# Kernel tuning notes

Hardware: AMD Instinct MI355X
Metric: run time of the kernel (lower is better)

## Reference

```python
import jax, jax.numpy as jnp
import numpy as np

EPS = 1e-5

def conv1x1(x, W, b):
    # x: [B,Cin,H,W], W: [Cout,Cin], b: [Cout] -> [B,Cout,H,W]
    return jnp.einsum('oc,bchw->bohw', W, x) + b[None, :, None, None]

def setup_inputs() -> dict:
    key = jax.random.key(0)
    ks = jax.random.split(key, 12)
    C, Ci = 256, 128
    B, Hh, Wh, Hl, Wl = 8, 32, 32, 64, 64
    sc = 1.0 / np.sqrt(C)
    sci = 1.0 / np.sqrt(Ci)
    return {
        'x_high': jax.random.normal(ks[0], (B, C, Hh, Wh), jnp.float32),
        'x_low':  jax.random.normal(ks[1], (B, C, Hl, Wl), jnp.float32),
        'Wg': jax.random.normal(ks[2], (Ci, C), jnp.float32) * sc,
        'bg': jax.random.normal(ks[3], (Ci,), jnp.float32) * 0.01,
        'Wt': jax.random.normal(ks[4], (Ci, C), jnp.float32) * sc,
        'bt': jax.random.normal(ks[5], (Ci,), jnp.float32) * 0.01,
        'Wp': jax.random.normal(ks[6], (Ci, C), jnp.float32) * sc,
        'bp': jax.random.normal(ks[7], (Ci,), jnp.float32) * 0.01,
        'Wz': jax.random.normal(ks[8], (C, Ci), jnp.float32) * sci,
        'bz': jax.random.normal(ks[9], (C,), jnp.float32) * 0.01,
        'gamma': jnp.ones((C,), jnp.float32),
        'beta': jnp.zeros((C,), jnp.float32),
    }

def reference(x_high, x_low, Wg, bg, Wt, bt, Wp, bp, Wz, bz, gamma, beta):
    B, C, Hl, Wl = x_low.shape
    Ci = Wg.shape[0]
    Nh = x_high.shape[2] * x_high.shape[3]
    Nl = Hl * Wl
    # 1x1 conv projections (pure channel GEMMs)
    g_x = conv1x1(x_high, Wg, bg).reshape(B, Ci, Nh).transpose(0, 2, 1)    # [B,Nh,Ci]
    theta_x = conv1x1(x_low, Wt, bt).reshape(B, Ci, Nl).transpose(0, 2, 1) # [B,Nl,Ci]
    phi_x = conv1x1(x_high, Wp, bp).reshape(B, Ci, Nh)                     # [B,Ci,Nh]
    # unnormalized attention (no softmax), scaled by number of key positions
    f = jnp.matmul(theta_x, phi_x)            # [B,Nl,Nh]
    y = jnp.matmul(f / Nh, g_x)               # [B,Nl,Ci]
    y = y.transpose(0, 2, 1).reshape(B, Ci, Hl, Wl)
    # W_z: 1x1 conv then GroupNorm(num_groups=1) -> layernorm over (C,H,W) per sample
    z = conv1x1(y, Wz, bz)                    # [B,C,Hl,Wl]
    mu = jnp.mean(z, axis=(1, 2, 3), keepdims=True)
    var = jnp.var(z, axis=(1, 2, 3), keepdims=True)
    z = (z - mu) * jax.lax.rsqrt(var + EPS)
    z = z * gamma[None, :, None, None] + beta[None, :, None, None]
    return z
```

## Files before the change

### kernel.cpp

```cpp
#include <hip/hip_runtime.h>
#include <hip/hip_bf16.h>

typedef __attribute__((ext_vector_type(8))) short bf16x8;
typedef __attribute__((ext_vector_type(4))) float f32x4;
typedef __attribute__((ext_vector_type(4))) unsigned short us4;
typedef __attribute__((ext_vector_type(8))) unsigned short us8;

#define MFMA(a, b, c) __builtin_amdgcn_mfma_f32_16x16x32_bf16(a, b, c, 0, 0, 0)

__device__ inline unsigned short f2bf(float f) {
  unsigned u = __builtin_bit_cast(unsigned, f);
  u += 0x7FFF + ((u >> 16) & 1);
  return (unsigned short)(u >> 16);
}
__device__ inline float bf2f(unsigned short s) {
  unsigned u = ((unsigned)s) << 16;
  return __builtin_bit_cast(float, u);
}
__device__ inline void gll16(const unsigned short* gsrc, unsigned short* ldst) {
  __builtin_amdgcn_global_load_lds(
      (const __attribute__((address_space(1))) unsigned int*)gsrc,
      (__attribute__((address_space(3))) unsigned int*)ldst, 16, 0, 0);
}

__global__ __launch_bounds__(256) void trans_cn(
    const float* __restrict__ src, unsigned short* __restrict__ dst, int N) {
  __shared__ float Ts[64][65];
  const int b = blockIdx.x, c0 = blockIdx.y * 64, n0 = blockIdx.z * 64;
  const int t = threadIdx.x;
  #pragma unroll
  for (int j = 0; j < 4; ++j) {
    int slot = t + j * 256;
    int c = slot >> 4, q = slot & 15;
    float4 v = *(const float4*)&src[((size_t)(b * 256 + c0 + c)) * N + n0 + q * 4];
    Ts[c][q * 4 + 0] = v.x; Ts[c][q * 4 + 1] = v.y;
    Ts[c][q * 4 + 2] = v.z; Ts[c][q * 4 + 3] = v.w;
  }
  __syncthreads();
  #pragma unroll
  for (int rr = 0; rr < 2; ++rr) {
    int n = rr * 32 + (t >> 3), gq = t & 7;
    us8 u;
    #pragma unroll
    for (int k = 0; k < 8; ++k) u[k] = f2bf(Ts[gq * 8 + k][n]);
    *(us8*)&dst[((size_t)(b * N + n0 + n)) * 256 + c0 + gq * 8] = u;
  }
}

__global__ __launch_bounds__(256) void cvt_w2(
    const float* __restrict__ A, const float* __restrict__ B,
    unsigned short* __restrict__ Ab, unsigned short* __restrict__ Bb) {
  int i = blockIdx.x * 256 + threadIdx.x;
  float4 a = *(const float4*)&A[i * 4];
  float4 b = *(const float4*)&B[i * 4];
  us4 ua, ub;
  ua[0] = f2bf(a.x); ua[1] = f2bf(a.y); ua[2] = f2bf(a.z); ua[3] = f2bf(a.w);
  ub[0] = f2bf(b.x); ub[1] = f2bf(b.y); ub[2] = f2bf(b.z); ub[3] = f2bf(b.w);
  *(us4*)&Ab[i * 4] = ua;
  *(us4*)&Bb[i * 4] = ub;
}

__global__ __launch_bounds__(256) void proj_mfma(
    const unsigned short* __restrict__ xhT,
    const unsigned short* __restrict__ Wpb, const float* __restrict__ bp,
    const unsigned short* __restrict__ Wgb, const float* __restrict__ bg,
    unsigned short* __restrict__ phi,
    unsigned short* __restrict__ gg) {
  __shared__ unsigned short Bs[64 * 256];
  __shared__ unsigned short As[2][128 * 64];
  const int b = blockIdx.x, n0 = blockIdx.y * 64;
  const int t = threadIdx.x, lane = t & 63;
  const int wid = t >> 6, wr = wid >> 1, wc = wid & 1;
  #pragma unroll
  for (int j = 0; j < 8; ++j) {
    int slot = t + j * 256;
    int r = slot >> 5, gq = slot & 31;
    gll16(xhT + ((size_t)(b * 1024 + n0 + r)) * 256 + (gq ^ (r & 7)) * 8,
          Bs + slot * 8);
  }
  f32x4 accP[4][2] = {};
  f32x4 accG[4][2] = {};
  for (int kt = 0; kt < 4; ++kt) {
    #pragma unroll
    for (int p = 0; p < 2; ++p) {
      const unsigned short* W = p ? Wgb : Wpb;
      #pragma unroll
      for (int j = 0; j < 4; ++j) {
        int slot = t + j * 256;
        int r = slot >> 3, gq = slot & 7;
        gll16(W + (size_t)r * 256 + kt * 64 + (gq ^ (r & 7)) * 8,
              As[p] + slot * 8);
      }
    }
    __syncthreads();
    #pragma unroll
    for (int ks = 0; ks < 2; ++ks) {
      bf16x8 bfr[2];
      #pragma unroll
      for (int fm = 0; fm < 2; ++fm) {
        int r = wc * 32 + fm * 16 + (lane & 15);
        int gc = kt * 8 + ks * 4 + (lane >> 4);
        bfr[fm] = *(const bf16x8*)&Bs[r * 256 + (gc ^ (r & 7)) * 8];
      }
      #pragma unroll
      for (int fo = 0; fo < 4; ++fo) {
        int r = wr * 64 + fo * 16 + (lane & 15);
        int ga = ks * 4 + (lane >> 4);
        bf16x8 ap = *(const bf16x8*)&As[0][r * 64 + (ga ^ (r & 7)) * 8];
        bf16x8 ag = *(const bf16x8*)&As[1][r * 64 + (ga ^ (r & 7)) * 8];
        accP[fo][0] = MFMA(ap, bfr[0], accP[fo][0]);
        accP[fo][1] = MFMA(ap, bfr[1], accP[fo][1]);
        accG[fo][0] = MFMA(ag, bfr[0], accG[fo][0]);
        accG[fo][1] = MFMA(ag, bfr[1], accG[fo][1]);
      }
    }
    __syncthreads();
  }
  #pragma unroll
  for (int fo = 0; fo < 4; ++fo) {
    #pragma unroll
    for (int q = 0; q < 4; ++q) {
      int i = wr * 64 + fo * 16 + (lane >> 4) * 4 + q;
      float vp = bp[i], vg = bg[i];
      #pragma unroll
      for (int fm = 0; fm < 2; ++fm) {
        int n = n0 + wc * 32 + fm * 16 + (lane & 15);
        size_t off = ((size_t)(b * 128 + i)) * 1024 + n;
        phi[off] = f2bf(accP[fo][fm][q] + vp);
        gg[off]  = f2bf(accG[fo][fm][q] + vg);
      }
    }
  }
}

__global__ __launch_bounds__(256) void mpart_mfma(
    const unsigned short* __restrict__ phi, const unsigned short* __restrict__ gg,
    float* __restrict__ Mpart) {
  __shared__ unsigned short ps[128 * 128];
  __shared__ unsigned short gs[128 * 128];
  const int b = blockIdx.x, kc = blockIdx.y;
  const int t = threadIdx.x, lane = t & 63;
  const int wid = t >> 6, wr = wid >> 1, wc = wid & 1;
  #pragma unroll
  for (int j = 0; j < 8; ++j) {
    int slot = t + j * 256;
    int r = slot >> 4, gq = slot & 15;
    size_t src = ((size_t)(b * 128 + r)) * 1024 + kc * 128 + (gq ^ (r & 7)) * 8;
    gll16(phi + src, ps + slot * 8);
    gll16(gg + src, gs + slot * 8);
  }
  __syncthreads();
  f32x4 acc[4][4] = {};
  #pragma unroll
  for (int ks = 0; ks < 4; ++ks) {
    bf16x8 av[4], bv[4];
    #pragma unroll
    for (int f = 0; f < 4; ++f) {
      int ra = wr * 64 + f * 16 + (lane & 15);
      int rb = wc * 64 + f * 16 + (lane & 15);
      int gc = ks * 4 + (lane >> 4);
      av[f] = *(const bf16x8*)&ps[ra * 128 + (gc ^ (ra & 7)) * 8];
      bv[f] = *(const bf16x8*)&gs[rb * 128 + (gc ^ (rb & 7)) * 8];
    }
    #pragma unroll
    for (int i = 0; i < 4; ++i)
      #pragma unroll
      for (int j2 = 0; j2 < 4; ++j2)
        acc[i][j2] = MFMA(av[i], bv[j2], acc[i][j2]);
  }
  float* mp = Mpart + ((size_t)(b * 8 + kc)) * 128 * 128;
  #pragma unroll
  for (int i = 0; i < 4; ++i)
    #pragma unroll
    for (int q = 0; q < 4; ++q) {
      int ii = wr * 64 + i * 16 + (lane >> 4) * 4 + q;
      #pragma unroll
      for (int j2 = 0; j2 < 4; ++j2) {
        int jj = wc * 64 + j2 * 16 + (lane & 15);
        mp[ii * 128 + jj] = acc[i][j2][q];
      }
    }
}

__global__ __launch_bounds__(256) void mreduce(
    const float* __restrict__ Mpart, float* __restrict__ M) {
  int i4 = blockIdx.x * 256 + threadIdx.x;
  int b = i4 >> 12, r4 = i4 & 4095;
  const float4* p = (const float4*)Mpart + (size_t)b * 8 * 4096 + r4;
  float4 s = {0.f, 0.f, 0.f, 0.f};
  #pragma unroll
  for (int kc = 0; kc < 8; ++kc) {
    float4 v = p[(size_t)kc * 4096];
    s.x += v.x; s.y += v.y; s.z += v.z; s.w += v.w;
  }
  const float sc = 1.0f / 1024.0f;
  s.x *= sc; s.y *= sc; s.z *= sc; s.w *= sc;
  ((float4*)M)[i4] = s;
}

__global__ __launch_bounds__(256) void mk_K(
    const float* __restrict__ M, const float* __restrict__ Wz,
    float* __restrict__ K) {
  const int b = blockIdx.x, o0 = blockIdx.y * 32;
  const int t = threadIdx.x;
  const int i = t & 127, og = (t >> 7) * 16;
  float acc[16] = {};
  const float* mrow = M + ((size_t)(b * 128 + i)) * 128;
  for (int j = 0; j < 128; j += 4) {
    float4 m4 = *(const float4*)&mrow[j];
    #pragma unroll
    for (int o = 0; o < 16; ++o) {
      float4 w4 = *(const float4*)&Wz[(o0 + og + o) * 128 + j];
      acc[o] += m4.x * w4.x + m4.y * w4.y + m4.z * w4.z + m4.w * w4.w;
    }
  }
  #pragma unroll
  for (int o = 0; o < 16; ++o)
    K[((size_t)(b * 256 + o0 + og + o)) * 128 + i] = acc[o];
}

__global__ __launch_bounds__(256) void mk_W2(
    const float* __restrict__ K, const float* __restrict__ Wt,
    const float* __restrict__ bt, const float* __restrict__ bz,
    unsigned short* __restrict__ W2b, float* __restrict__ b2) {
  __shared__ float Ks[32 * 128];
  const int b = blockIdx.x, o0 = blockIdx.y * 32;
  const int t = threadIdx.x;
  #pragma unroll
  for (int k = 0; k < 4; ++k) {
    int f = t + k * 256;
    int o = f >> 5, q = (f & 31) << 2;
    *(float4*)&Ks[o * 128 + q] = *(const float4*)&K[((size_t)(b * 256 + o0 + o)) * 128 + q];
  }
  __syncthreads();
  const int c = t;
  float acc[32] = {};
  for (int i = 0; i < 128; i += 4) {
    float w0 = Wt[(i + 0) * 256 + c];
    float w1 = Wt[(i + 1) * 256 + c];
    float w2 = Wt[(i + 2) * 256 + c];
    float w3 = Wt[(i + 3) * 256 + c];
    #pragma unroll
    for (int o = 0; o < 32; ++o) {
      float4 k4 = *(const float4*)&Ks[o * 128 + i];
      acc[o] += k4.x * w0 + k4.y * w1 + k4.z * w2 + k4.w * w3;
    }
  }
  #pragma unroll
  for (int o = 0; o < 32; ++o)
    W2b[((size_t)(b * 256 + o0 + o)) * 256 + c] = f2bf(acc[o]);
  if (t < 32) {
    float s = 0.f;
    for (int i = 0; i < 128; ++i) s += Ks[t * 128 + i] * bt[i];
    b2[b * 256 + o0 + t] = s + bz[o0 + t];
  }
}

__global__ __launch_bounds__(256) void mk_z_mfma(
    const unsigned short* __restrict__ xlT,
    const unsigned short* __restrict__ W2b,
    const float* __restrict__ b2,
    unsigned short* __restrict__ z,
    float* __restrict__ sums) {
  __shared__ unsigned short As[128 * 64];
  __shared__ unsigned short Bs[128 * 64];
  __shared__ float red[8];
  const int b = blockIdx.x, ot = blockIdx.y, mt = blockIdx.z;
  const int t = threadIdx.x, lane = t & 63;
  const int wid = t >> 6, wr = wid >> 1, wc = wid & 1;
  f32x4 acc[4][4] = {};
  for (int kt = 0; kt < 4; ++kt) {
    #pragma unroll
    for (int j = 0; j < 4; ++j) {
      int slot = t + j * 256;
      int r = slot >> 3, gq = slot & 7;
      int cg = kt * 64 + (gq ^ (r & 7)) * 8;
      gll16(W2b + ((size_t)(b * 256 + ot * 128 + r)) * 256 + cg, As + slot * 8);
      gll16(xlT + ((size_t)(b * 4096 + mt * 128 + r)) * 256 + cg, Bs + slot * 8);
    }
    __syncthreads();
    #pragma unroll
    for (int ks = 0; ks < 2; ++ks) {
      bf16x8 av[4], bv[4];
      #pragma unroll
      for (int f = 0; f < 4; ++f) {
        int ra = wr * 64 + f * 16 + (lane & 15);
        int rb = wc * 64 + f * 16 + (lane & 15);
        int gc = ks * 4 + (lane >> 4);
        av[f] = *(const bf16x8*)&As[ra * 64 + (gc ^ (ra & 7)) * 8];
        bv[f] = *(const bf16x8*)&Bs[rb * 64 + (gc ^ (rb & 7)) * 8];
      }
      #pragma unroll
      for (int i = 0; i < 4; ++i)
        #pragma unroll
        for (int j2 = 0; j2 < 4; ++j2)
          acc[i][j2] = MFMA(av[i], bv[j2], acc[i][j2]);
    }
    __syncthreads();
  }
  float ls = 0.f, ls2 = 0.f;
  #pragma unroll
  for (int i = 0; i < 4; ++i) {
    #pragma unroll
    for (int q = 0; q < 4; ++q) {
      int o = ot * 128 + wr * 64 + i * 16 + (lane >> 4) * 4 + q;
      float bias = b2[b * 256 + o];
      #pragma unroll
      for (int j2 = 0; j2 < 4; ++j2) {
        int m = mt * 128 + wc * 64 + j2 * 16 + (lane & 15);
        float v = acc[i][j2][q] + bias;
        z[((size_t)(b * 256 + o)) * 4096 + m] = f2bf(v);
        ls += v; ls2 += v * v;
      }
    }
  }
  #pragma unroll
  for (int off = 32; off > 0; off >>= 1) {
    ls  += __shfl_down(ls, off);
    ls2 += __shfl_down(ls2, off);
  }
  if ((t & 63) == 0) { red[wid * 2] = ls; red[wid * 2 + 1] = ls2; }
  __syncthreads();
  if (t == 0) {
    atomicAdd(&sums[b * 2 + 0], red[0] + red[2] + red[4] + red[6]);
    atomicAdd(&sums[b * 2 + 1], red[1] + red[3] + red[5] + red[7]);
  }
}

__global__ __launch_bounds__(256) void ln_out(
    const unsigned short* __restrict__ z, const float* __restrict__ sums,
    const float* __restrict__ gamma, const float* __restrict__ beta,
    float* __restrict__ out) {
  size_t i8 = (size_t)blockIdx.x * 256 + threadIdx.x;
  int b = (int)(i8 >> 17);
  int o = (int)((i8 >> 9) & 255);
  float s = sums[b * 2], s2 = sums[b * 2 + 1];
  const float invN = 1.0f / (256.0f * 4096.0f);
  float mu = s * invN;
  float var = s2 * invN - mu * mu;
  float rs = rsqrtf(var + 1e-5f);
  float ga = gamma[o] * rs;
  float be = beta[o] - mu * rs * gamma[o];
  us8 u = *(const us8*)&z[i8 * 8];
  float4 r0, r1;
  r0.x = bf2f(u[0]) * ga + be; r0.y = bf2f(u[1]) * ga + be;
  r0.z = bf2f(u[2]) * ga + be; r0.w = bf2f(u[3]) * ga + be;
  r1.x = bf2f(u[4]) * ga + be; r1.y = bf2f(u[5]) * ga + be;
  r1.z = bf2f(u[6]) * ga + be; r1.w = bf2f(u[7]) * ga + be;
  *(float4*)&out[i8 * 8] = r0;
  *(float4*)&out[i8 * 8 + 4] = r1;
}

extern "C" void kernel_launch(void* const* d_in, const int* in_sizes, int n_in,
                              void* d_out, int out_size, void* d_ws, size_t ws_size,
                              hipStream_t stream) {
  const float* xh    = (const float*)d_in[0];
  const float* xl    = (const float*)d_in[1];
  const float* Wg    = (const float*)d_in[2];
  const float* bg    = (const float*)d_in[3];
  const float* Wt    = (const float*)d_in[4];
  const float* bt    = (const float*)d_in[5];
  const float* Wp    = (const float*)d_in[6];
  const float* bp    = (const float*)d_in[7];
  const float* Wz    = (const float*)d_in[8];
  const float* bz    = (const float*)d_in[9];
  const float* gamma = (const float*)d_in[10];
  const float* beta  = (const float*)d_in[11];
  float* out = (float*)d_out;
  float* ws = (float*)d_ws;

  unsigned short* xhT  = (unsigned short*)(ws + 0);
  unsigned short* phi  = (unsigned short*)(ws + 1048576);
  unsigned short* gbuf = (unsigned short*)(ws + 1572864);
  float* Mpart = ws + 2097152;
  float* M     = ws + 3145728;
  float* K     = ws + 3276800;
  unsigned short* zbuf = (unsigned short*)(ws + 0);
  unsigned short* xlT  = (unsigned short*)(ws + 4194304);
  unsigned short* W2b  = (unsigned short*)(ws + 8388608);
  float* b2    = ws + 8650752;
  float* sums  = ws + 8652800;
  unsigned short* Wpb  = (unsigned short*)(ws + 8652816);
  unsigned short* Wgb  = (unsigned short*)(ws + 8669200);

  hipMemsetAsync(sums, 0, 16 * sizeof(float), stream);

  trans_cn<<<dim3(8, 4, 16), 256, 0, stream>>>(xh, xhT, 1024);
  trans_cn<<<dim3(8, 4, 64), 256, 0, stream>>>(xl, xlT, 4096);
  cvt_w2<<<32, 256, 0, stream>>>(Wp, Wg, Wpb, Wgb);
  proj_mfma<<<dim3(8, 16), 256, 0, stream>>>(xhT, Wpb, bp, Wgb, bg, phi, gbuf);
  mpart_mfma<<<dim3(8, 8), 256, 0, stream>>>(phi, gbuf, Mpart);
  mreduce<<<128, 256, 0, stream>>>(Mpart, M);
  mk_K<<<dim3(8, 8), 256, 0, stream>>>(M, Wz, K);
  mk_W2<<<dim3(8, 8), 256, 0, stream>>>(K, Wt, bt, bz, W2b, b2);
  mk_z_mfma<<<dim3(8, 2, 32), 256, 0, stream>>>(xlT, W2b, b2, zbuf, sums);
  ln_out<<<4096, 256, 0, stream>>>(zbuf, sums, gamma, beta, out);
}
```

Before: 219.0 us.

## Fuse fp32-to-bf16 transpose into projection and z GEMM tile loads

Removes the two standalone transpose/convert kernels for x_high and x_low. The projection and final z GEMM kernels now read the fp32 channel-major inputs directly, convert pairs of channels to packed bf16 and write them into swizzled LDS tiles. The z GEMM is also retiled so each block covers all 256 output channels for 64 spatial positions. This avoids writing and rereading bf16 copies of the large x_low tensor. In exchange, the loads become register-staged instead of async global-to-LDS, and each x_low tile is converted only once per block.

```diff
diff --git a/kernel.cpp b/kernel.cpp
--- a/kernel.cpp
+++ b/kernel.cpp
@@ -17,34 +17,13 @@
   unsigned u = ((unsigned)s) << 16;
   return __builtin_bit_cast(float, u);
 }
+__device__ inline unsigned pack2(float lo, float hi) {
+  return (unsigned)f2bf(lo) | ((unsigned)f2bf(hi) << 16);
+}
 __device__ inline void gll16(const unsigned short* gsrc, unsigned short* ldst) {
   __builtin_amdgcn_global_load_lds(
       (const __attribute__((address_space(1))) unsigned int*)gsrc,
       (__attribute__((address_space(3))) unsigned int*)ldst, 16, 0, 0);
-}
-
-__global__ __launch_bounds__(256) void trans_cn(
-    const float* __restrict__ src, unsigned short* __restrict__ dst, int N) {
-  __shared__ float Ts[64][65];
-  const int b = blockIdx.x, c0 = blockIdx.y * 64, n0 = blockIdx.z * 64;
-  const int t = threadIdx.x;
-  #pragma unroll
-  for (int j = 0; j < 4; ++j) {
-    int slot = t + j * 256;
-    int c = slot >> 4, q = slot & 15;
-    float4 v = *(const float4*)&src[((size_t)(b * 256 + c0 + c)) * N + n0 + q * 4];
-    Ts[c][q * 4 + 0] = v.x; Ts[c][q * 4 + 1] = v.y;
-    Ts[c][q * 4 + 2] = v.z; Ts[c][q * 4 + 3] = v.w;
-  }
-  __syncthreads();
-  #pragma unroll
-  for (int rr = 0; rr < 2; ++rr) {
-    int n = rr * 32 + (t >> 3), gq = t & 7;
-    us8 u;
-    #pragma unroll
-    for (int k = 0; k < 8; ++k) u[k] = f2bf(Ts[gq * 8 + k][n]);
-    *(us8*)&dst[((size_t)(b * N + n0 + n)) * 256 + c0 + gq * 8] = u;
-  }
 }
 
 __global__ __launch_bounds__(256) void cvt_w2(
@@ -60,8 +39,8 @@
   *(us4*)&Bb[i * 4] = ub;
 }
 
-__global__ __launch_bounds__(256) void proj_mfma(
-    const unsigned short* __restrict__ xhT,
+__global__ __launch_bounds__(256) void proj_f(
+    const float* __restrict__ xh,
     const unsigned short* __restrict__ Wpb, const float* __restrict__ bp,
     const unsigned short* __restrict__ Wgb, const float* __restrict__ bg,
     unsigned short* __restrict__ phi,
@@ -72,11 +51,21 @@
   const int t = threadIdx.x, lane = t & 63;
   const int wid = t >> 6, wr = wid >> 1, wc = wid & 1;
   #pragma unroll
-  for (int j = 0; j < 8; ++j) {
-    int slot = t + j * 256;
-    int r = slot >> 5, gq = slot & 31;
-    gll16(xhT + ((size_t)(b * 1024 + n0 + r)) * 256 + (gq ^ (r & 7)) * 8,
-          Bs + slot * 8);
+  for (int it = 0; it < 8; ++it) {
+    int s = it * 256 + t;
+    int nf = (s & 7) | ((s >> 10) << 3);
+    int c2 = (s >> 3) & 127;
+    const float* p = xh + ((size_t)(b * 256 + 2 * c2)) * 1024 + n0 + nf * 4;
+    float4 a = *(const float4*)p;
+    float4 bq = *(const float4*)(p + 1024);
+    const float* ap = (const float*)&a;
+    const float* bp2 = (const float*)&bq;
+    #pragma unroll
+    for (int i = 0; i < 4; ++i) {
+      int n = nf * 4 + i;
+      int col32 = (((c2 >> 2) ^ (n & 7)) << 2) | (c2 & 3);
+      ((unsigned*)Bs)[n * 128 + col32] = pack2(ap[i], bp2[i]);
+    }
   }
   f32x4 accP[4][2] = {};
   f32x4 accG[4][2] = {};
@@ -256,27 +245,43 @@
   }
 }
 
-__global__ __launch_bounds__(256) void mk_z_mfma(
-    const unsigned short* __restrict__ xlT,
+__global__ __launch_bounds__(256) void mk_z_f(
+    const float* __restrict__ xl,
     const unsigned short* __restrict__ W2b,
     const float* __restrict__ b2,
     unsigned short* __restrict__ z,
     float* __restrict__ sums) {
-  __shared__ unsigned short As[128 * 64];
-  __shared__ unsigned short Bs[128 * 64];
+  __shared__ unsigned short As[256 * 64];
+  __shared__ unsigned short Bs[64 * 64];
   __shared__ float red[8];
-  const int b = blockIdx.x, ot = blockIdx.y, mt = blockIdx.z;
+  const int b = blockIdx.x, m0 = blockIdx.y * 64;
   const int t = threadIdx.x, lane = t & 63;
-  const int wid = t >> 6, wr = wid >> 1, wc = wid & 1;
+  const int w = t >> 6;
   f32x4 acc[4][4] = {};
   for (int kt = 0; kt < 4; ++kt) {
     #pragma unroll
-    for (int j = 0; j < 4; ++j) {
+    for (int j = 0; j < 8; ++j) {
       int slot = t + j * 256;
       int r = slot >> 3, gq = slot & 7;
-      int cg = kt * 64 + (gq ^ (r & 7)) * 8;
-      gll16(W2b + ((size_t)(b * 256 + ot * 128 + r)) * 256 + cg, As + slot * 8);
-      gll16(xlT + ((size_t)(b * 4096 + mt * 128 + r)) * 256 + cg, Bs + slot * 8);
+      gll16(W2b + ((size_t)(b * 256 + r)) * 256 + kt * 64 + (gq ^ (r & 7)) * 8,
+            As + slot * 8);
+    }
+    #pragma unroll
+    for (int it = 0; it < 2; ++it) {
+      int s = it * 256 + t;
+      int mf = (s & 7) | ((s >> 8) << 3);
+      int c2 = (s >> 3) & 31;
+      const float* p = xl + ((size_t)(b * 256 + kt * 64 + 2 * c2)) * 4096 + m0 + mf * 4;
+      float4 a = *(const float4*)p;
+      float4 bq = *(const float4*)(p + 4096);
+      const float* ap = (const float*)&a;
+      const float* bp2 = (const float*)&bq;
+      #pragma unroll
+      for (int i = 0; i < 4; ++i) {
+        int m = mf * 4 + i;
+        int col32 = (((c2 >> 2) ^ (m & 7)) << 2) | (c2 & 3);
+        ((unsigned*)Bs)[m * 32 + col32] = pack2(ap[i], bp2[i]);
+      }
     }
     __syncthreads();
     #pragma unroll
@@ -284,8 +289,8 @@
       bf16x8 av[4], bv[4];
       #pragma unroll
       for (int f = 0; f < 4; ++f) {
-        int ra = wr * 64 + f * 16 + (lane & 15);
-        int rb = wc * 64 + f * 16 + (lane & 15);
+        int ra = w * 64 + f * 16 + (lane & 15);
+        int rb = f * 16 + (lane & 15);
         int gc = ks * 4 + (lane >> 4);
         av[f] = *(const bf16x8*)&As[ra * 64 + (gc ^ (ra & 7)) * 8];
         bv[f] = *(const bf16x8*)&Bs[rb * 64 + (gc ^ (rb & 7)) * 8];
@@ -303,11 +308,11 @@
   for (int i = 0; i < 4; ++i) {
     #pragma unroll
     for (int q = 0; q < 4; ++q) {
-      int o = ot * 128 + wr * 64 + i * 16 + (lane >> 4) * 4 + q;
+      int o = w * 64 + i * 16 + (lane >> 4) * 4 + q;
       float bias = b2[b * 256 + o];
       #pragma unroll
       for (int j2 = 0; j2 < 4; ++j2) {
-        int m = mt * 128 + wc * 64 + j2 * 16 + (lane & 15);
+        int m = m0 + j2 * 16 + (lane & 15);
         float v = acc[i][j2][q] + bias;
         z[((size_t)(b * 256 + o)) * 4096 + m] = f2bf(v);
         ls += v; ls2 += v * v;
@@ -319,7 +324,7 @@
     ls  += __shfl_down(ls, off);
     ls2 += __shfl_down(ls2, off);
   }
-  if ((t & 63) == 0) { red[wid * 2] = ls; red[wid * 2 + 1] = ls2; }
+  if ((t & 63) == 0) { red[w * 2] = ls; red[w * 2 + 1] = ls2; }
   __syncthreads();
   if (t == 0) {
     atomicAdd(&sums[b * 2 + 0], red[0] + red[2] + red[4] + red[6]);
@@ -369,30 +374,26 @@
   float* out = (float*)d_out;
   float* ws = (float*)d_ws;
 
-  unsigned short* xhT  = (unsigned short*)(ws + 0);
-  unsigned short* phi  = (unsigned short*)(ws + 1048576);
-  unsigned short* gbuf = (unsigned short*)(ws + 1572864);
-  float* Mpart = ws + 2097152;
-  float* M     = ws + 3145728;
-  float* K     = ws + 3276800;
+  unsigned short* phi  = (unsigned short*)(ws + 0);
+  unsigned short* gbuf = (unsigned short*)(ws + 524288);
+  float* Mpart = ws + 1048576;
+  float* M     = ws + 2097152;
+  float* K     = ws + 2228224;
   unsigned short* zbuf = (unsigned short*)(ws + 0);
-  unsigned short* xlT  = (unsigned short*)(ws + 4194304);
-  unsigned short* W2b  = (unsigned short*)(ws + 8388608);
-  float* b2    = ws + 8650752;
-  float* sums  = ws + 8652800;
-  unsigned short* Wpb  = (unsigned short*)(ws + 8652816);
-  unsigned short* Wgb  = (unsigned short*)(ws + 8669200);
+  unsigned short* W2b  = (unsigned short*)(ws + 4194304);
+  float* b2    = ws + 4456448;
+  float* sums  = ws + 4458496;
+  unsigned short* Wpb  = (unsigned short*)(ws + 4458512);
+  unsigned short* Wgb  = (unsigned short*)(ws + 4474896);
 
   hipMemsetAsync(sums, 0, 16 * sizeof(float), stream);
 
-  trans_cn<<<dim3(8, 4, 16), 256, 0, stream>>>(xh, xhT, 1024);
-  trans_cn<<<dim3(8, 4, 64), 256, 0, stream>>>(xl, xlT, 4096);
   cvt_w2<<<32, 256, 0, stream>>>(Wp, Wg, Wpb, Wgb);
-  proj_mfma<<<dim3(8, 16), 256, 0, stream>>>(xhT, Wpb, bp, Wgb, bg, phi, gbuf);
+  proj_f<<<dim3(8, 16), 256, 0, stream>>>(xh, Wpb, bp, Wgb, bg, phi, gbuf);
   mpart_mfma<<<dim3(8, 8), 256, 0, stream>>>(phi, gbuf, Mpart);
   mreduce<<<128, 256, 0, stream>>>(Mpart, M);
   mk_K<<<dim3(8, 8), 256, 0, stream>>>(M, Wz, K);
   mk_W2<<<dim3(8, 8), 256, 0, stream>>>(K, Wt, bt, bz, W2b, b2);
-  mk_z_mfma<<<dim3(8, 2, 32), 256, 0, stream>>>(xlT, W2b, b2, zbuf, sums);
+  mk_z_f<<<dim3(8, 64), 256, 0, stream>>>(xl, W2b, b2, zbuf, sums);
   ln_out<<<4096, 256, 0, stream>>>(zbuf, sums, gamma, beta, out);
 }
```

New measurement: 207.3 us. 5.3% less time.
